# Performance work log

Measured on AMD Instinct MI355X. Metric: run time of the kernel, lower is better.

The kernel has to match this reference:

```python
import jax, jax.numpy as jnp
import numpy as np

B, S, D, H, L = 2048, 23, 768, 8, 50
HD = D // H  # head dim = 96
NEG = -1e9


def setup_inputs() -> dict:
    key = jax.random.key(0)
    ks = jax.random.split(key, 9)
    sc = 0.02
    return {
        "cls_embeddings": jax.random.normal(ks[0], (B, S, D), jnp.float32),
        "exist_mask": jax.random.randint(ks[1], (B, S), 0, 2, jnp.int32),
        "missing_table": jax.random.normal(ks[2], (S, D), jnp.float32) * sc,
        "in_proj_w": jax.random.normal(ks[3], (3 * D, D), jnp.float32) * sc,
        "in_proj_b": jax.random.normal(ks[4], (3 * D,), jnp.float32) * sc,
        "out_proj_w": jax.random.normal(ks[5], (D, D), jnp.float32) * sc,
        "out_proj_b": jax.random.normal(ks[6], (D,), jnp.float32) * sc,
        "pred_w": jax.random.normal(ks[7], (L, D), jnp.float32) * sc,
        "pred_b": jax.random.normal(ks[8], (L,), jnp.float32) * sc,
    }


def reference(cls_embeddings, exist_mask, missing_table, in_proj_w, in_proj_b,
              out_proj_w, out_proj_b, pred_w, pred_b):
    exist = exist_mask.astype(bool)  # [B,S] True where section present
    # Build section_embeddings: BERT CLS where present, learned missing emb otherwise
    base = jnp.where(exist[..., None], cls_embeddings, missing_table[None])  # [B,S,D]

    # nn.MultiheadAttention: shared in_proj then split into q,k,v
    qkv = base @ in_proj_w.T + in_proj_b          # [B,S,3D]
    q, k, v = jnp.split(qkv, 3, axis=-1)
    q = q.reshape(B, S, H, HD) * (1.0 / np.sqrt(HD))
    k = k.reshape(B, S, H, HD)
    v = v.reshape(B, S, H, HD)

    # single-query attention per missing section over EXISTING sections only
    scores = jnp.einsum('bqhd,bkhd->bhqk', q, k)  # [B,H,S,S]
    scores = jnp.where(exist[:, None, None, :], scores, NEG)
    attn = jax.nn.softmax(scores, axis=-1)
    ctx = jnp.einsum('bhqk,bkhd->bqhd', attn, v).reshape(B, S, D)
    attn_out = ctx @ out_proj_w.T + out_proj_b    # [B,S,D]

    # existing sections keep their CLS embedding; if an EHR has NO existing
    # sections the original code skips it entirely (keeps missing embeddings)
    any_exist = exist.any(axis=1)[:, None, None]  # [B,1,1]
    keep = exist[..., None] | ~any_exist
    section_embeddings = jnp.where(keep, base, attn_out)

    document_embeddings = section_embeddings.mean(axis=1)  # [B,D]
    logits = document_embeddings @ pred_w.T + pred_b       # [B,L]
    return logits
```

## Files before the change

### kernel.cpp

```cpp
#include <hip/hip_runtime.h>
#include <hip/hip_bf16.h>


typedef unsigned short u16;
typedef unsigned int u32;
typedef __attribute__((ext_vector_type(8))) short sh8;
typedef __attribute__((ext_vector_type(4))) float f32x4;

#define BB 2048
#define SS 23
#define DD 768
#define HH 8
#define HDIM 96
#define LL 50
#define NN 1024
#define NCAP 26624
#define MTILES 208

#define G_GATHER 26624
#define G_DOC    (G_GATHER + 6144)
#define G_GROW   (G_DOC + 552)
#define G_WFOLD  (G_GROW + 600)
#define G_LOG    (G_WFOLD + 50)

__device__ __forceinline__ u16 f2bf(float f) {
  u32 u = __float_as_uint(f);
  u32 r = (u + 0x7fffu + ((u >> 16) & 1u)) >> 16;
  return (u16)r;
}
__device__ __forceinline__ float bf2f(u16 h) {
  return __uint_as_float(((u32)h) << 16);
}

__device__ __forceinline__ void gld16(const void* g, void* l) {
  __builtin_amdgcn_global_load_lds((const __attribute__((address_space(1))) void*)g,
                                   (__attribute__((address_space(3))) void*)l, 16, 0, 0);
}

__global__ __launch_bounds__(256) void prep1_kernel(const int* __restrict__ exist,
                                                    const float* __restrict__ inw,
                                                    const float* __restrict__ inb,
                                                    const float* __restrict__ mt,
                                                    int* __restrict__ ex_off,
                                                    int* __restrict__ rowmap,
                                                    u16* __restrict__ Bcomb,
                                                    float* __restrict__ biasc,
                                                    float* __restrict__ qmf,
                                                    float* __restrict__ Wfold) {
  const int idx = blockIdx.x;
  const int t = threadIdx.x;
  if (idx == 0) {
    __shared__ int wtot[4];
    int tot = 0;
    for (int j = 0; j < 8; ++j) {
      const int b = t * 8 + j;
      for (int s = 0; s < SS; ++s) tot += (exist[b * SS + s] != 0);
    }
    const int lane = t & 63, w = t >> 6;
    int v = tot;
    for (int off = 1; off < 64; off <<= 1) {
      int n = __shfl_up(v, off, 64);
      if (lane >= off) v += n;
    }
    if (lane == 63) wtot[w] = v;
    __syncthreads();
    int wbase = 0;
    for (int i = 0; i < w; ++i) wbase += wtot[i];
    int base = wbase + v - tot;
    for (int j = 0; j < 8; ++j) {
      const int b = t * 8 + j;
      for (int s = 0; s < SS; ++s)
        if (exist[b * SS + s]) {
          if (base < NCAP) rowmap[base] = b * SS + s;
          ++base;
        }
      ex_off[b + 1] = base;
    }
    if (t == 0) ex_off[0] = 0;
  } else if (idx < 289) {
    const int i = ((idx - 1) * 256 + t) * 8;
    const float* src = inw + (size_t)2 * DD * DD;
    float4 a = *(const float4*)(src + i);
    float4 b = *(const float4*)(src + i + 4);
    uint4 o;
    o.x = (u32)f2bf(a.x) | ((u32)f2bf(a.y) << 16);
    o.y = (u32)f2bf(a.z) | ((u32)f2bf(a.w) << 16);
    o.z = (u32)f2bf(b.x) | ((u32)f2bf(b.y) << 16);
    o.w = (u32)f2bf(b.z) | ((u32)f2bf(b.w) << 16);
    *(uint4*)((u16*)Bcomb + i) = o;
  } else if (idx < 358) {
    const int q69 = idx - 289;
    const int s = q69 / 3;
    const int o = (q69 % 3) * 256 + t;
    const float* mrow = mt + s * DD;
    const float* wrow = inw + (size_t)o * DD;
    float acc = 0.f;
    for (int d = 0; d < DD; d += 4) {
      float4 a = *(const float4*)(mrow + d);
      float4 b = *(const float4*)(wrow + d);
      acc += a.x * b.x + a.y * b.y + a.z * b.z + a.w * b.w;
    }
    qmf[s * DD + o] = (acc + inb[o]) * 0.10206207261596575f;
  } else if (idx == 358) {
    for (int i = t; i < NN; i += 256) biasc[i] = (i < DD) ? inb[1536 + i] : 0.f;
  } else {
    const int i4 = (idx - 359) * 256 + t;
    if (i4 < (LL * DD) / 4) {
      float4 z = {0.f, 0.f, 0.f, 0.f};
      *(float4*)(Wfold + i4 * 4) = z;
    }
  }
}

__global__ __launch_bounds__(256) void prep2_kernel(const float* __restrict__ qmf,
                                                    const float* __restrict__ inw,
                                                    const float* __restrict__ inb,
                                                    const float* __restrict__ pw,
                                                    const float* __restrict__ pb,
                                                    const float* __restrict__ outw,
                                                    const float* __restrict__ outb,
                                                    const float* __restrict__ mt,
                                                    const float* __restrict__ cls,
                                                    const int* __restrict__ exist,
                                                    const int* __restrict__ ex_off,
                                                    const int* __restrict__ rowmap,
                                                    u16* __restrict__ Bcomb,
                                                    float* __restrict__ biasc,
                                                    float* __restrict__ Wfold,
                                                    float* __restrict__ boutdot,
                                                    float* __restrict__ logits0,
                                                    u16* __restrict__ Xex,
                                                    float* __restrict__ doc_acc) {
  const int idx = blockIdx.x;
  const int t = threadIdx.x;
  if (idx < G_GATHER) {
    const int r = idx;
    if (r >= ex_off[BB]) return;
    const int m = rowmap[r];
    if (t < 192) {
      const int d0 = t * 4;
      float4 v = *(const float4*)(cls + (size_t)m * DD + d0);
      ushort4 pk;
      pk.x = f2bf(v.x); pk.y = f2bf(v.y); pk.z = f2bf(v.z); pk.w = f2bf(v.w);
      *(ushort4*)(Xex + (size_t)r * DD + d0) = pk;
    }
  } else if (idx < G_DOC) {
    const int id = idx - G_GATHER;
    const int b = id / 3;
    const int d = (id % 3) * 256 + t;
    const float* cb = cls + (size_t)b * SS * DD + d;
    float acc = 0.f;
    for (int s = 0; s < SS; ++s)
      if (exist[b * SS + s]) acc += cb[(size_t)s * DD];
    doc_acc[(size_t)b * DD + d] = acc;
  } else if (idx < G_GROW) {
    const int id = idx - G_DOC;
    const int r = id / 3, chunk = id - r * 3;
    const int s = r >> 3, h = r & 7;
    const int Dc = chunk * 256 + t;
    const float* q = qmf + s * DD + h * HDIM;
    const float* wk = inw + (size_t)(DD + h * HDIM) * DD + Dc;
    float acc = 0.f;
    for (int d = 0; d < HDIM; ++d)
      acc += q[d] * wk[(size_t)d * DD];
    Bcomb[(size_t)(DD + r) * DD + Dc] = f2bf(acc);
    if (chunk == 0 && t == 0) {
      float bb = 0.f;
      const float* bk = inb + DD + h * HDIM;
      for (int d = 0; d < HDIM; ++d) bb += q[d] * bk[d];
      biasc[DD + r] = bb;
    }
  } else if (idx < G_WFOLD) {
    const int id = idx - G_GROW;
    const int l = id / 12, rem = id % 12;
    const int din = (rem % 3) * 256 + t;
    const int dc0 = (rem / 3) * 192;
    const float* pwl = pw + (size_t)l * DD;
    const float* ow = outw + (size_t)dc0 * DD + din;
    float acc = 0.f;
#pragma unroll 8
    for (int j = 0; j < 192; ++j)
      acc += pwl[dc0 + j] * ow[(size_t)j * DD];
    atomicAdd(&Wfold[(size_t)l * DD + din], acc);
  } else {
    __shared__ float red[2][256];
    const int l = idx - G_WFOLD;
    float pbd = 0.f, plz = 0.f;
    for (int d = t; d < DD; d += 256) {
      const float pv = pw[(size_t)l * DD + d];
      pbd += pv * outb[d];
      float ms = 0.f;
      for (int s = 0; s < SS; ++s) ms += mt[s * DD + d];
      plz += pv * ms;
    }
    red[0][t] = pbd; red[1][t] = plz;
    __syncthreads();
    for (int s = 128; s > 0; s >>= 1) {
      if (t < s) { red[0][t] += red[0][t + s]; red[1][t] += red[1][t + s]; }
      __syncthreads();
    }
    if (t == 0) { boutdot[l] = red[0][0]; logits0[l] = red[1][0] * (1.f / 23.f) + pb[l]; }
  }
}

__global__ __launch_bounds__(256, 2)
void gemm_bt_kernel(const u16* __restrict__ A, const u16* __restrict__ Bw,
                    const float* __restrict__ bias, u16* __restrict__ Cc,
                    const int* __restrict__ rows_ptr, int N) {
  constexpr int K = 768;
  __shared__ u16 lA[128 * 64];
  __shared__ u16 lB[128 * 64];
  const int m0 = blockIdx.y * 128;
  if (m0 >= rows_ptr[0]) return;
  const int n0 = blockIdx.x * 128;
  const int t = threadIdx.x;
  const int w = t >> 6, l = t & 63;
  const int wr = (w >> 1) * 64, wc = (w & 1) * 64;
  const int r16 = l & 15, kg = l >> 4;

  f32x4 acc[4][4] = {};

  const int srow = t >> 3;
  const int scol = (t & 7) * 8;
  const u16* gA = A + (size_t)(m0 + srow) * K + scol;
  const u16* gB = Bw + (size_t)(n0 + srow) * K + scol;
  u16* lAp = lA + t * 8;
  u16* lBp = lB + t * 8;

  for (int kt = 0; kt < K; kt += 64) {
#pragma unroll
    for (int i = 0; i < 4; ++i) {
      gld16(gA + (size_t)i * 32 * K + kt, lAp + i * 2048);
      gld16(gB + (size_t)i * 32 * K + kt, lBp + i * 2048);
    }
    __syncthreads();
#pragma unroll
    for (int kk = 0; kk < 2; ++kk) {
      sh8 af[4], bfr[4];
      const int kc = kk * 32 + kg * 8;
#pragma unroll
      for (int m = 0; m < 4; ++m) af[m] = *(const sh8*)(lA + (wr + m * 16 + r16) * 64 + kc);
#pragma unroll
      for (int n = 0; n < 4; ++n) bfr[n] = *(const sh8*)(lB + (wc + n * 16 + r16) * 64 + kc);
#pragma unroll
      for (int m = 0; m < 4; ++m)
#pragma unroll
        for (int n = 0; n < 4; ++n)
          acc[m][n] = __builtin_amdgcn_mfma_f32_16x16x32_bf16(af[m], bfr[n], acc[m][n], 0, 0, 0);
    }
    __syncthreads();
  }

#pragma unroll
  for (int m = 0; m < 4; ++m) {
    const int row0 = m0 + wr + m * 16 + kg * 4;
#pragma unroll
    for (int n = 0; n < 4; ++n) {
      const int col = n0 + wc + n * 16 + r16;
      const float bv = bias[col];
#pragma unroll
      for (int j = 0; j < 4; ++j)
        Cc[(size_t)(row0 + j) * N + col] = f2bf(acc[m][n][j] + bv);
    }
  }
}

__global__ __launch_bounds__(256) void attn_final_kernel(const u16* __restrict__ VS,
                                                         const int* __restrict__ exist,
                                                         const int* __restrict__ ex_off,
                                                         const float* __restrict__ doc_acc,
                                                         const float* __restrict__ pw,
                                                         const float* __restrict__ pb,
                                                         const float* __restrict__ Wfold,
                                                         const float* __restrict__ boutdot,
                                                         const float* __restrict__ logits0,
                                                         float* __restrict__ out) {
  const int b = blockIdx.x, t = threadIdx.x;
  __shared__ float sc[SS * HH][25];
  __shared__ float psum[HH][25];
  __shared__ float ctxL[DD];
  __shared__ int mil[SS], cnts[2];
  if (t == 0) {
    int ne = 0, nm = 0;
    for (int s = 0; s < SS; ++s) {
      if (exist[b * SS + s]) ne++; else mil[nm++] = s;
    }
    cnts[0] = ne; cnts[1] = nm;
  }
  __syncthreads();
  const int nE = cnts[0], nM = cnts[1];
  if (nE == 0) {
    if (t < LL) out[(size_t)b * LL + t] = logits0[t];
    return;
  }
  const size_t e0 = (size_t)ex_off[b];

  if (nM > 0) {
    const int ee = t & 31, ig = t >> 5;
    for (int i0 = 0; i0 < nM; i0 += 8) {
      const int i = i0 + ig;
      if (ee < nE && i < nM) {
        sh8 v = *(const sh8*)(VS + (e0 + ee) * NN + DD + mil[i] * 8);
#pragma unroll
        for (int h = 0; h < HH; ++h) sc[i * HH + h][ee] = bf2f((u16)v[h]);
      }
    }
    __syncthreads();

    if (t < nM * HH) {
      float* row = sc[t];
      float mx = row[0];
      for (int e = 1; e < nE; ++e) mx = fmaxf(mx, row[e]);
      float sum = 0.f;
      for (int e = 0; e < nE; ++e) { float p = __expf(row[e] - mx); row[e] = p; sum += p; }
      float inv = 1.f / sum;
      for (int e = 0; e < nE; ++e) row[e] *= inv;
    }
    __syncthreads();

    {
      const int h = t >> 5, e2 = t & 31;
      if (e2 < nE) {
        float a = 0.f;
        for (int i = 0; i < nM; ++i) a += sc[i * HH + h][e2];
        psum[h][e2] = a;
      }
    }
    __syncthreads();

    for (int d = t; d < DD; d += 256) {
      const int h = d / HDIM;
      float acc = 0.f;
      for (int e = 0; e < nE; ++e)
        acc += psum[h][e] * bf2f(VS[(e0 + e) * NN + d]);
      ctxL[d] = acc;
    }
    __syncthreads();
  }

  const int w = t >> 6, lane = t & 63;
  const int d0 = lane * 12;
  const float* db = doc_acc + (size_t)b * DD + d0;
  float docv[12];
  *(float4*)(docv)     = *(const float4*)(db);
  *(float4*)(docv + 4) = *(const float4*)(db + 4);
  *(float4*)(docv + 8) = *(const float4*)(db + 8);
  float ctxv[12];
  if (nM > 0) {
#pragma unroll
    for (int j = 0; j < 12; ++j) ctxv[j] = ctxL[d0 + j];
  }
  for (int l = w; l < LL; l += 4) {
    const float* pwl = pw + (size_t)l * DD + d0;
    float acc = 0.f;
    if (nM > 0) {
      const float* wfl = Wfold + (size_t)l * DD + d0;
#pragma unroll
      for (int j = 0; j < 12; ++j) acc += docv[j] * pwl[j] + ctxv[j] * wfl[j];
    } else {
#pragma unroll
      for (int j = 0; j < 12; ++j) acc += docv[j] * pwl[j];
    }
#pragma unroll
    for (int m = 1; m < 64; m <<= 1) acc += __shfl_xor(acc, m, 64);
    if (lane == 0)
      out[(size_t)b * LL + l] = (acc + (float)nM * boutdot[l]) * (1.f / 23.f) + pb[l];
  }
}

extern "C" void kernel_launch(void* const* d_in, const int* in_sizes, int n_in,
                              void* d_out, int out_size, void* d_ws, size_t ws_size,
                              hipStream_t stream) {
  const float* cls  = (const float*)d_in[0];
  const int*   exm  = (const int*)d_in[1];
  const float* mt   = (const float*)d_in[2];
  const float* inw  = (const float*)d_in[3];
  const float* inb  = (const float*)d_in[4];
  const float* outw = (const float*)d_in[5];
  const float* outb = (const float*)d_in[6];
  const float* pw   = (const float*)d_in[7];
  const float* pb   = (const float*)d_in[8];
  float* out = (float*)d_out;

  char* ws = (char*)d_ws;
  size_t off = 0;
  auto alloc = [&](size_t bytes) {
    size_t cur = (off + 255) & ~(size_t)255;
    off = cur + bytes;
    return ws + cur;
  };
  int*   ex_off  = (int*)alloc((BB + 1) * sizeof(int));
  int*   rowmap  = (int*)alloc((size_t)NCAP * sizeof(int));
  float* qmf     = (float*)alloc((size_t)SS * DD * 4);
  u16*   Bcomb   = (u16*)alloc((size_t)NN * DD * 2);
  float* biasc   = (float*)alloc((size_t)NN * 4);
  float* Wfold   = (float*)alloc((size_t)LL * DD * 4);
  float* boutdot = (float*)alloc((size_t)LL * 4);
  float* logits0 = (float*)alloc((size_t)LL * 4);
  float* doc_acc = (float*)alloc((size_t)BB * DD * 4);
  u16*   Xex     = (u16*)alloc((size_t)NCAP * DD * 2);
  u16*   VS      = (u16*)alloc((size_t)NCAP * NN * 2);

  prep1_kernel<<<397, 256, 0, stream>>>(exm, inw, inb, mt, ex_off, rowmap, Bcomb,
                                        biasc, qmf, Wfold);
  prep2_kernel<<<G_LOG, 256, 0, stream>>>(qmf, inw, inb, pw, pb, outw, outb, mt, cls,
                                          exm, ex_off, rowmap, Bcomb, biasc, Wfold,
                                          boutdot, logits0, Xex, doc_acc);
  gemm_bt_kernel<<<dim3(NN / 128, MTILES), 256, 0, stream>>>(Xex, Bcomb, biasc, VS,
                                                             ex_off + BB, NN);
  attn_final_kernel<<<BB, 256, 0, stream>>>(VS, exm, ex_off, doc_acc, pw, pb, Wfold,
                                            boutdot, logits0, out);
}
```

Before: 389.9 us.

## Fuse CLS gather with doc sum per batch and remap GEMM tiles per XCD

The per-row gather into the bf16 GEMM input and the separate per-batch document-sum pass are merged into one block per batch. That block reads each present CLS row once, writes the bf16 copy and accumulates the masked sum, so the rowmap table and the second read of cls are gone. The prefix scan now writes only per-batch offsets. The GEMM launch becomes 1D with a block-index remap so that the eight N-tiles of one M-tile land on the same XCD for L2 reuse of the A rows, and the prep branches are reordered so the heavier work blocks come first.

```diff
diff --git a/kernel.cpp b/kernel.cpp
--- a/kernel.cpp
+++ b/kernel.cpp
@@ -17,11 +17,10 @@
 #define NCAP 26624
 #define MTILES 208
 
-#define G_GATHER 26624
-#define G_DOC    (G_GATHER + 6144)
-#define G_GROW   (G_DOC + 552)
-#define G_WFOLD  (G_GROW + 600)
-#define G_LOG    (G_WFOLD + 50)
+#define G_WFOLD  600
+#define G_GROW   (G_WFOLD + 552)
+#define G_GATHER (G_GROW + 2048)
+#define G_LOG    (G_GATHER + 50)
 
 __device__ __forceinline__ u16 f2bf(float f) {
   u32 u = __float_as_uint(f);
@@ -42,7 +41,6 @@
                                                     const float* __restrict__ inb,
                                                     const float* __restrict__ mt,
                                                     int* __restrict__ ex_off,
-                                                    int* __restrict__ rowmap,
                                                     u16* __restrict__ Bcomb,
                                                     float* __restrict__ biasc,
                                                     float* __restrict__ qmf,
@@ -51,10 +49,14 @@
   const int t = threadIdx.x;
   if (idx == 0) {
     __shared__ int wtot[4];
+    int c[8];
     int tot = 0;
     for (int j = 0; j < 8; ++j) {
       const int b = t * 8 + j;
-      for (int s = 0; s < SS; ++s) tot += (exist[b * SS + s] != 0);
+      int cc = 0;
+      for (int s = 0; s < SS; ++s) cc += (exist[b * SS + s] != 0);
+      tot += cc;
+      c[j] = tot;
     }
     const int lane = t & 63, w = t >> 6;
     int v = tot;
@@ -66,16 +68,8 @@
     __syncthreads();
     int wbase = 0;
     for (int i = 0; i < w; ++i) wbase += wtot[i];
-    int base = wbase + v - tot;
-    for (int j = 0; j < 8; ++j) {
-      const int b = t * 8 + j;
-      for (int s = 0; s < SS; ++s)
-        if (exist[b * SS + s]) {
-          if (base < NCAP) rowmap[base] = b * SS + s;
-          ++base;
-        }
-      ex_off[b + 1] = base;
-    }
+    const int excl = wbase + v - tot;
+    for (int j = 0; j < 8; ++j) ex_off[t * 8 + j + 1] = excl + c[j];
     if (t == 0) ex_off[0] = 0;
   } else if (idx < 289) {
     const int i = ((idx - 1) * 256 + t) * 8;
@@ -123,7 +117,6 @@
                                                     const float* __restrict__ cls,
                                                     const int* __restrict__ exist,
                                                     const int* __restrict__ ex_off,
-                                                    const int* __restrict__ rowmap,
                                                     u16* __restrict__ Bcomb,
                                                     float* __restrict__ biasc,
                                                     float* __restrict__ Wfold,
@@ -133,28 +126,19 @@
                                                     float* __restrict__ doc_acc) {
   const int idx = blockIdx.x;
   const int t = threadIdx.x;
-  if (idx < G_GATHER) {
-    const int r = idx;
-    if (r >= ex_off[BB]) return;
-    const int m = rowmap[r];
-    if (t < 192) {
-      const int d0 = t * 4;
-      float4 v = *(const float4*)(cls + (size_t)m * DD + d0);
-      ushort4 pk;
-      pk.x = f2bf(v.x); pk.y = f2bf(v.y); pk.z = f2bf(v.z); pk.w = f2bf(v.w);
-      *(ushort4*)(Xex + (size_t)r * DD + d0) = pk;
-    }
-  } else if (idx < G_DOC) {
-    const int id = idx - G_GATHER;
-    const int b = id / 3;
-    const int d = (id % 3) * 256 + t;
-    const float* cb = cls + (size_t)b * SS * DD + d;
+  if (idx < G_WFOLD) {
+    const int l = idx / 12, rem = idx % 12;
+    const int din = (rem % 3) * 256 + t;
+    const int dc0 = (rem / 3) * 192;
+    const float* pwl = pw + (size_t)l * DD;
+    const float* ow = outw + (size_t)dc0 * DD + din;
     float acc = 0.f;
-    for (int s = 0; s < SS; ++s)
-      if (exist[b * SS + s]) acc += cb[(size_t)s * DD];
-    doc_acc[(size_t)b * DD + d] = acc;
+#pragma unroll 8
+    for (int j = 0; j < 192; ++j)
+      acc += pwl[dc0 + j] * ow[(size_t)j * DD];
+    atomicAdd(&Wfold[(size_t)l * DD + din], acc);
   } else if (idx < G_GROW) {
-    const int id = idx - G_DOC;
+    const int id = idx - G_WFOLD;
     const int r = id / 3, chunk = id - r * 3;
     const int s = r >> 3, h = r & 7;
     const int Dc = chunk * 256 + t;
@@ -170,21 +154,31 @@
       for (int d = 0; d < HDIM; ++d) bb += q[d] * bk[d];
       biasc[DD + r] = bb;
     }
-  } else if (idx < G_WFOLD) {
-    const int id = idx - G_GROW;
-    const int l = id / 12, rem = id % 12;
-    const int din = (rem % 3) * 256 + t;
-    const int dc0 = (rem / 3) * 192;
-    const float* pwl = pw + (size_t)l * DD;
-    const float* ow = outw + (size_t)dc0 * DD + din;
-    float acc = 0.f;
-#pragma unroll 8
-    for (int j = 0; j < 192; ++j)
-      acc += pwl[dc0 + j] * ow[(size_t)j * DD];
-    atomicAdd(&Wfold[(size_t)l * DD + din], acc);
+  } else if (idx < G_GATHER) {
+    const int b = idx - G_GROW;
+    if (t < 192) {
+      const int d0 = t * 4;
+      int r = ex_off[b];
+      float a0 = 0.f, a1 = 0.f, a2 = 0.f, a3 = 0.f;
+      const float* cb = cls + (size_t)b * SS * DD + d0;
+      for (int s = 0; s < SS; ++s) {
+        if (exist[b * SS + s]) {
+          float4 v = *(const float4*)(cb + (size_t)s * DD);
+          a0 += v.x; a1 += v.y; a2 += v.z; a3 += v.w;
+          if (r < NCAP) {
+            ushort4 pk;
+            pk.x = f2bf(v.x); pk.y = f2bf(v.y); pk.z = f2bf(v.z); pk.w = f2bf(v.w);
+            *(ushort4*)(Xex + (size_t)r * DD + d0) = pk;
+          }
+          ++r;
+        }
+      }
+      float4 outv = {a0, a1, a2, a3};
+      *(float4*)(doc_acc + (size_t)b * DD + d0) = outv;
+    }
   } else {
     __shared__ float red[2][256];
-    const int l = idx - G_WFOLD;
+    const int l = idx - G_GATHER;
     float pbd = 0.f, plz = 0.f;
     for (int d = t; d < DD; d += 256) {
       const float pv = pw[(size_t)l * DD + d];
@@ -210,9 +204,14 @@
   constexpr int K = 768;
   __shared__ u16 lA[128 * 64];
   __shared__ u16 lB[128 * 64];
-  const int m0 = blockIdx.y * 128;
+  const int i = blockIdx.x;
+  const int xcd = i & 7;
+  const int j = i >> 3;
+  const int m_tile = xcd + ((j >> 3) << 3);
+  const int n_tile = j & 7;
+  const int m0 = m_tile * 128;
   if (m0 >= rows_ptr[0]) return;
-  const int n0 = blockIdx.x * 128;
+  const int n0 = n_tile * 128;
   const int t = threadIdx.x;
   const int w = t >> 6, l = t & 63;
   const int wr = (w >> 1) * 64, wc = (w & 1) * 64;
@@ -229,9 +228,9 @@
 
   for (int kt = 0; kt < K; kt += 64) {
 #pragma unroll
-    for (int i = 0; i < 4; ++i) {
-      gld16(gA + (size_t)i * 32 * K + kt, lAp + i * 2048);
-      gld16(gB + (size_t)i * 32 * K + kt, lBp + i * 2048);
+    for (int ii = 0; ii < 4; ++ii) {
+      gld16(gA + (size_t)ii * 32 * K + kt, lAp + ii * 2048);
+      gld16(gB + (size_t)ii * 32 * K + kt, lBp + ii * 2048);
     }
     __syncthreads();
 #pragma unroll
@@ -259,8 +258,8 @@
       const int col = n0 + wc + n * 16 + r16;
       const float bv = bias[col];
 #pragma unroll
-      for (int j = 0; j < 4; ++j)
-        Cc[(size_t)(row0 + j) * N + col] = f2bf(acc[m][n][j] + bv);
+      for (int jj = 0; jj < 4; ++jj)
+        Cc[(size_t)(row0 + jj) * N + col] = f2bf(acc[m][n][jj] + bv);
     }
   }
 }
@@ -390,7 +389,6 @@
     return ws + cur;
   };
   int*   ex_off  = (int*)alloc((BB + 1) * sizeof(int));
-  int*   rowmap  = (int*)alloc((size_t)NCAP * sizeof(int));
   float* qmf     = (float*)alloc((size_t)SS * DD * 4);
   u16*   Bcomb   = (u16*)alloc((size_t)NN * DD * 2);
   float* biasc   = (float*)alloc((size_t)NN * 4);
@@ -401,13 +399,13 @@
   u16*   Xex     = (u16*)alloc((size_t)NCAP * DD * 2);
   u16*   VS      = (u16*)alloc((size_t)NCAP * NN * 2);
 
-  prep1_kernel<<<397, 256, 0, stream>>>(exm, inw, inb, mt, ex_off, rowmap, Bcomb,
-                                        biasc, qmf, Wfold);
+  prep1_kernel<<<397, 256, 0, stream>>>(exm, inw, inb, mt, ex_off, Bcomb, biasc,
+                                        qmf, Wfold);
   prep2_kernel<<<G_LOG, 256, 0, stream>>>(qmf, inw, inb, pw, pb, outw, outb, mt, cls,
-                                          exm, ex_off, rowmap, Bcomb, biasc, Wfold,
+                                          exm, ex_off, Bcomb, biasc, Wfold,
                                           boutdot, logits0, Xex, doc_acc);
-  gemm_bt_kernel<<<dim3(NN / 128, MTILES), 256, 0, stream>>>(Xex, Bcomb, biasc, VS,
-                                                             ex_off + BB, NN);
+  gemm_bt_kernel<<<MTILES * (NN / 128), 256, 0, stream>>>(Xex, Bcomb, biasc, VS,
+                                                          ex_off + BB, NN);
   attn_final_kernel<<<BB, 256, 0, stream>>>(VS, exm, ex_off, doc_acc, pw, pb, Wfold,
                                             boutdot, logits0, out);
 }
```

New measurement: 342.5 us. 12.2% less time.
